# Optimization experiments

Measured on AMD Instinct MI355X. Metric: run time of the kernel, lower is better.

## Reference

```python
import jax, jax.numpy as jnp
import numpy as np

N = 50000      # nodes
E = 100000     # edges
D_IN = 16      # raw node feature dim
K = 16         # RWSE steps
H = 32         # node_hidden_dim (== D_IN + K for residual)
ED = H * H     # edge_input_dim, must be H*H for NNConv reshape


def _seg_sum(x, idx, n):
    return jax.ops.segment_sum(x, idx, num_segments=n)


def setup_inputs() -> dict:
    key = jax.random.key(0)
    ks = jax.random.split(key, 14)
    s = 0.02
    return {
        "n_feat": jax.random.normal(ks[0], (N, D_IN), jnp.float32),
        "e_feat": jax.random.normal(ks[1], (E, ED), jnp.float32),
        "src": jax.random.randint(ks[2], (E,), 0, N, jnp.int32),
        "dst": jax.random.randint(ks[3], (E,), 0, N, jnp.int32),
        "edge_proj_w": jax.random.normal(ks[4], (ED, ED), jnp.float32) * s,
        "edge_proj_b": jnp.zeros((ED,), jnp.float32),
        "gate_w": jax.random.normal(ks[5], (ED, 1), jnp.float32) * s,
        "gate_b": jnp.zeros((1,), jnp.float32),
        "lin0_w": jax.random.normal(ks[6], (D_IN + K, H), jnp.float32) * s,
        "lin0_b": jnp.zeros((H,), jnp.float32),
        "conv_bias": jnp.zeros((H,), jnp.float32),
        "message_w": jax.random.normal(ks[7], (2 * H, H), jnp.float32) * s,
        "message_b": jnp.zeros((H,), jnp.float32),
        "subgraph_w": jax.random.normal(ks[8], (2 * H, H), jnp.float32) * s,
        "subgraph_b": jnp.zeros((H,), jnp.float32),
    }


def reference(n_feat, e_feat, src, dst, edge_proj_w, edge_proj_b, gate_w, gate_b,
              lin0_w, lin0_b, conv_bias, message_w, message_b, subgraph_w, subgraph_b):
    ones_e = jnp.ones((E,), n_feat.dtype)
    deg = _seg_sum(ones_e, dst, N)                 # in-degree (adj row-sum)
    degc = jnp.where(deg == 0, 1.0, deg)

    # --- RWSE (sparse equivalent of dense adj @ x recursion) ---
    x = degc
    cols = [x]
    for _ in range(K - 1):
        x = _seg_sum(x[src], dst, N) / degc
        cols.append(x)
    rwse = jnp.stack(cols, axis=1)                 # (N, K)

    nf = jnp.concatenate([n_feat, rwse], axis=-1)  # (N, D_IN+K)
    init = nf
    out = jax.nn.relu(nf @ lin0_w + lin0_b)        # (N, H)

    # --- edge-conditioned weights (EnhancedEdgeNetwork), same every step ---
    proj = jax.nn.relu(e_feat @ edge_proj_w + edge_proj_b)   # (E, H*H)
    gate = jax.nn.sigmoid(e_feat @ gate_w + gate_b)          # (E, 1)
    W = (proj * gate).reshape(E, H, H)                       # (E, H, H)

    # --- NNConv mean-aggregation message passing (num_steps//2 iters) ---
    for _ in range(3):
        msg = jnp.einsum('eh,eho->eo', out[src], W)          # gather + transform
        neigh = _seg_sum(msg, dst, N) / degc[:, None]        # scatter-mean
        m = jax.nn.relu(neigh + out + conv_bias)             # residual (identity) + bias
        out = jnp.concatenate([m, out], axis=1) @ message_w + message_b

    # --- copy_u/mean group pooling + subgraph projection ---
    group = _seg_sum(out[src], dst, N) / degc[:, None]
    out = jnp.concatenate([out, group], axis=1) @ subgraph_w + subgraph_b
    return out + init
```

## Files before the change

### kernel.cpp

```cpp
#include <hip/hip_runtime.h>
#include <hip/hip_bf16.h>

typedef unsigned short u16;
typedef unsigned int   u32;
typedef __bf16 bf16x8 __attribute__((ext_vector_type(8)));
typedef float  f32x4  __attribute__((ext_vector_type(4)));

#define AS1 __attribute__((address_space(1)))
#define AS3 __attribute__((address_space(3)))

__device__ __forceinline__ u16 f2bf(float f){
    u32 u = __float_as_uint(f);
    u32 r = u + 0x7fffu + ((u>>16)&1u);
    return (u16)(r>>16);
}
__device__ __forceinline__ float bf2f(u16 u){ return __uint_as_float(((u32)u)<<16); }

__global__ void k_deg(const int* __restrict__ dst, float* __restrict__ degb, int E){
    int e = blockIdx.x*256 + threadIdx.x;
    if (e < E) atomicAdd(&degb[dst[e]], 1.0f);
}

__global__ void k_degc(float* __restrict__ invdeg, float* __restrict__ rw0, int n){
    int v = blockIdx.x*256 + threadIdx.x;
    if (v < n){
        float c = invdeg[v];
        if (c == 0.f) c = 1.f;
        invdeg[v] = 1.f/c;
        rw0[v] = c*c;
    }
}

__global__ void k_rwse(const float* __restrict__ cur, float* __restrict__ nxt,
                       const float* __restrict__ invdeg, const int* __restrict__ src,
                       const int* __restrict__ dst, int E){
    int e = blockIdx.x*256 + threadIdx.x;
    if (e < E){
        int s = src[e];
        atomicAdd(&nxt[dst[e]], cur[s]*invdeg[s]);
    }
}

__global__ void k_finalize(const float* __restrict__ nfeat, const float* __restrict__ rw,
                           const float* __restrict__ invdeg,
                           const float* __restrict__ lw, const float* __restrict__ lb,
                           float* __restrict__ out0, int n){
    __shared__ float lwl[1024];
    __shared__ float lbl[32];
    __shared__ float nfl[8][32];
    int tid = threadIdx.x;
    for (int i = tid; i < 1024; i += 256) lwl[i] = lw[i];
    if (tid < 32) lbl[tid] = lb[tid];
    int slot = tid>>5, o = tid&31;
    int v = blockIdx.x*8 + slot;
    float nfv = 0.f;
    if (v < n){
        nfv = (o < 16) ? nfeat[(size_t)v*16 + o]
                       : rw[(size_t)(o-16)*n + v]*invdeg[v];
    }
    nfl[slot][o] = nfv;
    __syncthreads();
    if (v < n){
        float a = lbl[o];
        #pragma unroll
        for (int j = 0; j < 32; j++) a += nfl[slot][j]*lwl[j*32+o];
        out0[(size_t)v*32 + o] = a > 0.f ? a : 0.f;
    }
}

__global__ void k_transpose(const float* __restrict__ w, u16* __restrict__ wt){
    __shared__ float t[32][33];
    int bx = blockIdx.x & 31, by = blockIdx.x >> 5;
    int x = threadIdx.x & 31, y = threadIdx.x >> 5;
    #pragma unroll
    for (int i = 0; i < 32; i += 8)
        t[y+i][x] = w[(size_t)(by*32 + y + i)*1024 + bx*32 + x];
    __syncthreads();
    #pragma unroll
    for (int i = 0; i < 32; i += 8)
        wt[(size_t)(bx*32 + y + i)*1024 + by*32 + x] = f2bf(t[x][y+i]);
}

__global__ __launch_bounds__(256) void k_prep(
    const float* __restrict__ A, const float* __restrict__ gw,
    const float* __restrict__ gb, u16* __restrict__ Abf,
    float* __restrict__ gate, int E)
{
    __shared__ f32x4 gwl[256];
    const int tid = threadIdx.x;
    const int wave = tid>>6, lane = tid&63;
    gwl[tid] = ((const f32x4*)gw)[tid];
    __syncthreads();
    const int row = blockIdx.x*4 + wave;
    if (row >= E) return;
    const f32x4* ar = (const f32x4*)(A + (size_t)row*1024);
    ushort4* br = (ushort4*)(Abf + (size_t)row*1024);
    float g = 0.f;
    #pragma unroll
    for (int j = 0; j < 4; j++){
        const int idx = j*64 + lane;
        f32x4 v = ar[idx];
        f32x4 w4 = gwl[idx];
        g += v.x*w4.x + v.y*w4.y + v.z*w4.z + v.w*w4.w;
        ushort4 o;
        o.x = f2bf(v.x); o.y = f2bf(v.y); o.z = f2bf(v.z); o.w = f2bf(v.w);
        br[idx] = o;
    }
    #pragma unroll
    for (int m = 32; m >= 1; m >>= 1) g += __shfl_xor(g, m);
    if (lane == 0) gate[row] = 1.f/(1.f + __expf(-(g + gb[0])));
}

__global__ __launch_bounds__(256) void k_gemm(
    const u16* __restrict__ A, const u16* __restrict__ BT,
    const float* __restrict__ bias, const float* __restrict__ gate,
    u16* __restrict__ Wout, int E)
{
    __shared__ __align__(16) u16 lds_a[3*128*32];
    __shared__ __align__(16) u16 lds_b[3*128*32];
    __shared__ float gate_lds[128];
    __shared__ float bias_lds[128];

    const int tid  = threadIdx.x;
    const int wave = tid>>6, lane = tid&63;
    const int wm = wave>>1, wn = wave&1;
    const int ql = lane>>4, rl = lane&15;

    const int id  = blockIdx.x;
    const int xcd = id & 7;
    const int s   = id >> 3;
    const int nb  = s & 7;
    const int mb  = (s >> 3)*8 + xcd;
    const int MBtot = (E + 127) >> 7;
    if (mb >= MBtot) return;
    const int m0 = mb<<7, n0 = nb<<7;

    if (tid < 128){
        const int row = m0 + tid;
        gate_lds[tid] = gate[row < E ? row : E-1];
    } else {
        bias_lds[tid-128] = bias[n0 + tid - 128];
    }
    __syncthreads();

#define STAGE(buf, kk)                                                      \
    {                                                                       \
        const int k0s = (kk);                                               \
        _Pragma("unroll")                                                   \
        for (int j=0;j<2;j++){                                              \
            const int cb = (j*4 + wave)*64;                                 \
            const int ci = cb + lane;                                       \
            const int m  = ci & 127, q = ci >> 7;                           \
            int row = m0 + m; if (row >= E) row = E-1;                      \
            const u16* ga = A + (size_t)row*1024 + k0s + q*8;               \
            __builtin_amdgcn_global_load_lds((const AS1 void*)ga,           \
                (AS3 void*)&lds_a[(buf)*4096 + ci*8], 16, 0, 0);            \
            const u16* gB = BT + (size_t)(n0 + m)*1024 + (k0s + q*8);       \
            __builtin_amdgcn_global_load_lds((const AS1 void*)gB,           \
                (AS3 void*)&lds_b[(buf)*4096 + ci*8], 16, 0, 0);            \
        }                                                                   \
    }

    f32x4 acc[4][4];
    #pragma unroll
    for (int i=0;i<4;i++)
    #pragma unroll
        for (int j=0;j<4;j++) acc[i][j] = (f32x4){0.f,0.f,0.f,0.f};

    STAGE(0, 0)
    STAGE(1, 32)
    asm volatile("s_waitcnt vmcnt(4)" ::: "memory");
    __builtin_amdgcn_s_barrier();

    int bc = 0;
    for (int t = 0; t < 32; ++t){
        if (t + 2 < 32){
            int bs = bc + 2; if (bs >= 3) bs -= 3;
            STAGE(bs, (t+2)*32)
        }

        const u16* la = &lds_a[bc*4096];
        const u16* lb = &lds_b[bc*4096];
        bf16x8 af[4], bfr[4];
        #pragma unroll
        for (int tt=0;tt<4;tt++){
            af[tt]  = *(const bf16x8*)&la[(ql*128 + wm*64 + tt*16 + rl)*8];
            bfr[tt] = *(const bf16x8*)&lb[(ql*128 + wn*64 + tt*16 + rl)*8];
        }
        #pragma unroll
        for (int mt=0;mt<4;mt++)
        #pragma unroll
            for (int nt=0;nt<4;nt++)
                acc[mt][nt] = __builtin_amdgcn_mfma_f32_16x16x32_bf16(af[mt], bfr[nt], acc[mt][nt], 0,0,0);

        if (t + 2 < 32)      asm volatile("s_waitcnt vmcnt(4)" ::: "memory");
        else if (t + 1 < 32) asm volatile("s_waitcnt vmcnt(0)" ::: "memory");
        if (t + 1 < 32) __builtin_amdgcn_s_barrier();

        bc = bc + 1; if (bc >= 3) bc -= 3;
    }
#undef STAGE

    float bcol[4];
    #pragma unroll
    for (int nt=0;nt<4;nt++) bcol[nt] = bias_lds[wn*64 + nt*16 + rl];

    #pragma unroll
    for (int mt=0;mt<4;mt++){
        const int rloc0 = wm*64 + mt*16 + ql*4;
        #pragma unroll
        for (int r=0;r<4;r++){
            const int row = m0 + rloc0 + r;
            if (row < E){
                const float g = gate_lds[rloc0 + r];
                u16* wrow = Wout + (size_t)row*1024 + n0 + wn*64 + rl;
                #pragma unroll
                for (int nt=0;nt<4;nt++){
                    float v = acc[mt][nt][r] + bcol[nt];
                    v = v > 0.f ? v : 0.f;
                    wrow[nt*16] = f2bf(v*g);
                }
            }
        }
    }
}

__global__ void k_msg(const float* __restrict__ outc, const u16* __restrict__ W,
                      const int* __restrict__ src, const int* __restrict__ dst,
                      float* __restrict__ neigh, int E)
{
    __shared__ float xl[8][32];
    const int tid = threadIdx.x, slot = tid>>5, o = tid&31;
    const int e = blockIdx.x*8 + slot;
    int d = 0;
    if (e < E){
        d = dst[e];
        xl[slot][o] = outc[(size_t)src[e]*32 + o];
    }
    __syncthreads();
    if (e < E){
        const float* x = xl[slot];
        const u16* wr = W + (size_t)e*1024 + o;
        float acc = 0.f;
        #pragma unroll
        for (int h = 0; h < 32; h++)
            acc += x[h]*bf2f(wr[h*32]);
        atomicAdd(&neigh[(size_t)d*32 + o], acc);
    }
}

__global__ void k_node(const float* __restrict__ neigh, const float* __restrict__ invdeg,
                       const float* __restrict__ outc, const float* __restrict__ cb,
                       const float* __restrict__ mw, const float* __restrict__ mb,
                       float* __restrict__ outn, int n)
{
    __shared__ float mwl[2048];
    __shared__ float cat[8][64];
    int tid = threadIdx.x;
    for (int i = tid; i < 2048; i += 256) mwl[i] = mw[i];
    int slot = tid>>5, o = tid&31;
    int v = blockIdx.x*8 + slot;
    if (v < n){
        float ov = outc[(size_t)v*32 + o];
        float m = neigh[(size_t)v*32 + o]*invdeg[v] + ov + cb[o];
        m = m > 0.f ? m : 0.f;
        cat[slot][o] = m;
        cat[slot][32+o] = ov;
    }
    __syncthreads();
    if (v < n){
        float a = mb[o];
        #pragma unroll
        for (int j = 0; j < 64; j++) a += cat[slot][j]*mwl[j*32+o];
        outn[(size_t)v*32 + o] = a;
    }
}

__global__ void k_group(const float* __restrict__ outc, const int* __restrict__ src,
                        const int* __restrict__ dst, float* __restrict__ grp, int E)
{
    int tid = threadIdx.x, slot = tid>>5, o = tid&31;
    int e = blockIdx.x*8 + slot;
    if (e < E)
        atomicAdd(&grp[(size_t)dst[e]*32 + o], outc[(size_t)src[e]*32 + o]);
}

__global__ void k_final(const float* __restrict__ outc, const float* __restrict__ grp,
                        const float* __restrict__ invdeg, const float* __restrict__ sw,
                        const float* __restrict__ sb, const float* __restrict__ nfeat,
                        const float* __restrict__ rw,
                        float* __restrict__ dout, int n)
{
    __shared__ float swl[2048];
    __shared__ float cat[8][64];
    int tid = threadIdx.x;
    for (int i = tid; i < 2048; i += 256) swl[i] = sw[i];
    int slot = tid>>5, o = tid&31;
    int v = blockIdx.x*8 + slot;
    float iv = 0.f;
    if (v < n){
        iv = invdeg[v];
        cat[slot][o] = outc[(size_t)v*32 + o];
        cat[slot][32+o] = grp[(size_t)v*32 + o]*iv;
    }
    __syncthreads();
    if (v < n){
        float a = sb[o];
        #pragma unroll
        for (int j = 0; j < 64; j++) a += cat[slot][j]*swl[j*32+o];
        float initv = (o < 16) ? nfeat[(size_t)v*16 + o]
                               : rw[(size_t)(o-16)*n + v]*iv;
        dout[(size_t)v*32 + o] = a + initv;
    }
}

extern "C" void kernel_launch(void* const* d_in, const int* in_sizes, int n_in,
                              void* d_out, int out_size, void* d_ws, size_t ws_size,
                              hipStream_t stream)
{
    const float* n_feat = (const float*)d_in[0];
    const float* e_feat = (const float*)d_in[1];
    const int*   src    = (const int*)d_in[2];
    const int*   dst    = (const int*)d_in[3];
    const float* epw    = (const float*)d_in[4];
    const float* epb    = (const float*)d_in[5];
    const float* gw     = (const float*)d_in[6];
    const float* gb     = (const float*)d_in[7];
    const float* l0w    = (const float*)d_in[8];
    const float* l0b    = (const float*)d_in[9];
    const float* cb     = (const float*)d_in[10];
    const float* mw     = (const float*)d_in[11];
    const float* mbp    = (const float*)d_in[12];
    const float* sw     = (const float*)d_in[13];
    const float* sb     = (const float*)d_in[14];

    const int N = in_sizes[0] / 16;
    const int E = in_sizes[2];

    char* w = (char*)d_ws;
    float* invdeg = (float*)w;  w += (size_t)N*4;
    float* rw     = (float*)w;  w += (size_t)16*N*4;
    float* out_a  = (float*)w;  w += (size_t)32*N*4;
    float* out_b  = (float*)w;  w += (size_t)32*N*4;
    float* neigh  = (float*)w;  w += (size_t)32*N*4;
    u16*   wtb    = (u16*)w;    w += (size_t)1024*1024*2;
    u16*   abf    = (u16*)w;    w += (size_t)E*1024*2;
    float* gatev  = (float*)w;  w += (size_t)E*4;
    u16*   wout   = (u16*)w;

    hipMemsetAsync(invdeg, 0, (size_t)N*4, stream);
    hipMemsetAsync(rw, 0, (size_t)16*N*4, stream);

    const int EB  = (E + 255)/256, NB = (N + 255)/256;
    const int EB8 = (E + 7)/8,    NB8 = (N + 7)/8;

    k_deg<<<EB,256,0,stream>>>(dst, invdeg, E);
    k_degc<<<NB,256,0,stream>>>(invdeg, rw, N);
    for (int t = 0; t < 15; t++)
        k_rwse<<<EB,256,0,stream>>>(rw + (size_t)t*N, rw + (size_t)(t+1)*N, invdeg, src, dst, E);
    k_finalize<<<NB8,256,0,stream>>>(n_feat, rw, invdeg, l0w, l0b, out_a, N);

    k_transpose<<<1024,256,0,stream>>>(epw, wtb);
    k_prep<<<(E+3)/4,256,0,stream>>>(e_feat, gw, gb, abf, gatev, E);

    const int MBtot = (E + 127)/128;
    const int grid  = ((MBtot + 7)/8)*64;
    k_gemm<<<grid,256,0,stream>>>(abf, wtb, epb, gatev, wout, E);

    float* cur = out_a; float* nxt = out_b;
    for (int it = 0; it < 3; it++){
        hipMemsetAsync(neigh, 0, (size_t)32*N*4, stream);
        k_msg<<<EB8,256,0,stream>>>(cur, wout, src, dst, neigh, E);
        k_node<<<NB8,256,0,stream>>>(neigh, invdeg, cur, cb, mw, mbp, nxt, N);
        float* tmp = cur; cur = nxt; nxt = tmp;
    }

    hipMemsetAsync(neigh, 0, (size_t)32*N*4, stream);
    k_group<<<EB8,256,0,stream>>>(cur, src, dst, neigh, E);
    k_final<<<NB8,256,0,stream>>>(cur, neigh, invdeg, sw, sb, n_feat, rw, (float*)d_out, N);

    (void)n_in; (void)out_size; (void)ws_size;
}
```

Measured before the change: 1.415 ms.

## Use row-major XOR-swizzled LDS layout for GEMM tiles with precomputed load pointers

Changes the global-to-LDS staging so each lane loads four consecutive 16-byte chunks of a row, which makes global reads more contiguous per row. The LDS tile becomes row-major with an XOR swizzle on the chunk index, meant to avoid bank conflicts when fragments are read. Global pointers are precomputed once and advanced by 32 elements per stage, replacing per-stage address arithmetic. The swizzle on the staging side and the read side must agree, otherwise results are wrong.

```diff
diff --git a/kernel.cpp b/kernel.cpp
--- a/kernel.cpp
+++ b/kernel.cpp
@@ -143,23 +143,35 @@
     }
     __syncthreads();
 
-#define STAGE(buf, kk)                                                      \
+    const int ci0 = (0*4 + wave)*64 + lane;
+    const int ci1 = (1*4 + wave)*64 + lane;
+    const int mA0 = ci0>>2, cA0 = ci0&3, qA0 = cA0 ^ ((mA0>>1)&3);
+    const int mA1 = ci1>>2, cA1 = ci1&3, qA1 = cA1 ^ ((mA1>>1)&3);
+    int rA0 = m0 + mA0; if (rA0 >= E) rA0 = E-1;
+    int rA1 = m0 + mA1; if (rA1 >= E) rA1 = E-1;
+    const u16* pA0 = A + (size_t)rA0*1024 + qA0*8;
+    const u16* pA1 = A + (size_t)rA1*1024 + qA1*8;
+    const u16* pB0 = BT + (size_t)(n0 + mA0)*1024 + qA0*8;
+    const u16* pB1 = BT + (size_t)(n0 + mA1)*1024 + qA1*8;
+    const int cb0 = (0*4 + wave)*64;
+    const int cb1 = (1*4 + wave)*64;
+
+#define STAGE(buf)                                                          \
     {                                                                       \
-        const int k0s = (kk);                                               \
-        _Pragma("unroll")                                                   \
-        for (int j=0;j<2;j++){                                              \
-            const int cb = (j*4 + wave)*64;                                 \
-            const int ci = cb + lane;                                       \
-            const int m  = ci & 127, q = ci >> 7;                           \
-            int row = m0 + m; if (row >= E) row = E-1;                      \
-            const u16* ga = A + (size_t)row*1024 + k0s + q*8;               \
-            __builtin_amdgcn_global_load_lds((const AS1 void*)ga,           \
-                (AS3 void*)&lds_a[(buf)*4096 + ci*8], 16, 0, 0);            \
-            const u16* gB = BT + (size_t)(n0 + m)*1024 + (k0s + q*8);       \
-            __builtin_amdgcn_global_load_lds((const AS1 void*)gB,           \
-                (AS3 void*)&lds_b[(buf)*4096 + ci*8], 16, 0, 0);            \
-        }                                                                   \
-    }
+        __builtin_amdgcn_global_load_lds((const AS1 void*)pA0,              \
+            (AS3 void*)&lds_a[(buf)*4096 + cb0*8], 16, 0, 0);               \
+        __builtin_amdgcn_global_load_lds((const AS1 void*)pB0,              \
+            (AS3 void*)&lds_b[(buf)*4096 + cb0*8], 16, 0, 0);               \
+        __builtin_amdgcn_global_load_lds((const AS1 void*)pA1,              \
+            (AS3 void*)&lds_a[(buf)*4096 + cb1*8], 16, 0, 0);               \
+        __builtin_amdgcn_global_load_lds((const AS1 void*)pB1,              \
+            (AS3 void*)&lds_b[(buf)*4096 + cb1*8], 16, 0, 0);               \
+        pA0 += 32; pA1 += 32; pB0 += 32; pB1 += 32;                         \
+    }
+
+    const int xr = (rl>>1)&3;
+    const int a_off = (wm*64 + rl)*32 + (ql ^ xr)*8;
+    const int b_off = (wn*64 + rl)*32 + (ql ^ xr)*8;
 
     f32x4 acc[4][4];
     #pragma unroll
@@ -167,8 +179,8 @@
     #pragma unroll
         for (int j=0;j<4;j++) acc[i][j] = (f32x4){0.f,0.f,0.f,0.f};
 
-    STAGE(0, 0)
-    STAGE(1, 32)
+    STAGE(0)
+    STAGE(1)
     asm volatile("s_waitcnt vmcnt(4)" ::: "memory");
     __builtin_amdgcn_s_barrier();
 
@@ -176,7 +188,7 @@
     for (int t = 0; t < 32; ++t){
         if (t + 2 < 32){
             int bs = bc + 2; if (bs >= 3) bs -= 3;
-            STAGE(bs, (t+2)*32)
+            STAGE(bs)
         }
 
         const u16* la = &lds_a[bc*4096];
@@ -184,8 +196,8 @@
         bf16x8 af[4], bfr[4];
         #pragma unroll
         for (int tt=0;tt<4;tt++){
-            af[tt]  = *(const bf16x8*)&la[(ql*128 + wm*64 + tt*16 + rl)*8];
-            bfr[tt] = *(const bf16x8*)&lb[(ql*128 + wn*64 + tt*16 + rl)*8];
+            af[tt]  = *(const bf16x8*)&la[a_off + tt*512];
+            bfr[tt] = *(const bf16x8*)&lb[b_off + tt*512];
         }
         #pragma unroll
         for (int mt=0;mt<4;mt++)
```

After: 1.264 ms. -10.6%, faster.
